# Kernel optimization log

Hardware: AMD Instinct MI355X
Metric: run time of the kernel (lower is better)

The kernel has to match this reference:

```python
import jax, jax.numpy as jnp
import numpy as np

T, H, E, I, K = 2048, 2048, 16, 512, 2
ROUTED_SCALE = 1.5   # config.moe_router_scaling_factor
SWIGLU_LIMIT = 7.0   # config.swiglu_limits[layer_id]


def setup_inputs() -> dict:
    key = jax.random.key(0)
    k1, k2, k3, k4, k5 = jax.random.split(key, 5)
    hidden_states = jax.random.normal(k1, (T, H), jnp.float32)
    gate_w = jax.random.normal(k2, (E, H), jnp.float32) * 0.02
    router_bias = jax.random.normal(k3, (E,), jnp.float32) * 0.01
    w13 = jax.random.normal(k4, (E, 2 * I, H), jnp.float32) * 0.02  # [gate; up] fused
    w2 = jax.random.normal(k5, (E, H, I), jnp.float32) * 0.02
    return {"hidden_states": hidden_states, "gate_w": gate_w,
            "router_bias": router_bias, "w13": w13, "w2": w2, "top_k": K}


def reference(hidden_states, gate_w, router_bias, w13, w2, top_k):
    n_tok = hidden_states.shape[0]
    n_exp = gate_w.shape[0]
    # fp32 gate (need_fp32_gate=True)
    router_logits = hidden_states.astype(jnp.float32) @ gate_w.T          # [T, E]
    scores = jax.nn.sigmoid(router_logits)
    # correction bias only affects expert choice, not the combine weights
    _, topk_ids = jax.lax.top_k(scores + router_bias[None, :], top_k)     # [T, K]
    topk_w = jnp.take_along_axis(scores, topk_ids, axis=1)                # [T, K]
    topk_w = topk_w / jnp.sum(topk_w, axis=1, keepdims=True)              # renormalize
    topk_w = topk_w * ROUTED_SCALE
    # scatter routing weights into dense per-expert combine weights [T, E]
    comb = jnp.zeros((n_tok, n_exp), jnp.float32)
    comb = comb.at[jnp.arange(n_tok)[:, None], topk_ids].add(topk_w)
    # expert SwiGLU MLPs, dense over experts (zero combine weight == not routed)
    gu = jnp.einsum('th,eoh->teo', hidden_states, w13)                    # [T, E, 2I]
    g, u = jnp.split(gu, 2, axis=-1)
    g = jnp.minimum(g, SWIGLU_LIMIT)                                      # gemm1_clamp_limit
    u = jnp.clip(u, -SWIGLU_LIMIT, SWIGLU_LIMIT)
    act = g * jax.nn.sigmoid(g) * u                                       # silu(gate) * up
    expert_out = jnp.einsum('tei,ehi->teh', act, w2)                      # [T, E, H]
    return jnp.einsum('teh,te->th', expert_out, comb)                     # [T, H]
```

## Files before the change

### kernel.cpp

```cpp
#include <hip/hip_runtime.h>
#include <hip/hip_bf16.h>
#include <math.h>

#define T_TOK 2048
#define H_DIM 2048
#define E_EXP 16
#define I_DIM 512
#define TWO_I 1024
#define ROUTED_SCALE 1.5f
#define SWIGLU_LIMIT 7.0f

#define BM 64
#define KC 64
#define PADMAX 5120
#define MAX_TILES 80

typedef __attribute__((ext_vector_type(8))) short bf16x8;
typedef __attribute__((ext_vector_type(4))) float f32x4;
typedef unsigned short u16;

__device__ inline u16 f2bf(float f) {
    return __builtin_bit_cast(u16, __float2bfloat16(f));
}
__device__ inline bf16x8 pack8(float4 a, float4 b) {
    bf16x8 v;
    v[0] = (short)f2bf(a.x); v[1] = (short)f2bf(a.y);
    v[2] = (short)f2bf(a.z); v[3] = (short)f2bf(a.w);
    v[4] = (short)f2bf(b.x); v[5] = (short)f2bf(b.y);
    v[6] = (short)f2bf(b.z); v[7] = (short)f2bf(b.w);
    return v;
}

#define SWZ(row, k) ((row) * 64 + ((k) ^ (((row) & 7) << 3)))

__global__ __launch_bounds__(256) void router_kernel(
    const float* __restrict__ hs, const float* __restrict__ gw,
    const float* __restrict__ bias, int* cnt, int* tok_list, float* w_list,
    u16* __restrict__ hs_bf)
{
    int wave = threadIdx.x >> 6;
    int lane = threadIdx.x & 63;
    int t = blockIdx.x * 4 + wave;
    if (t >= T_TOK) return;
    const float* x = hs + (size_t)t * H_DIM;

    float acc[E_EXP];
#pragma unroll
    for (int e = 0; e < E_EXP; ++e) acc[e] = 0.f;

#pragma unroll 2
    for (int c = 0; c < 8; ++c) {
        int col = c * 256 + lane * 4;
        float4 xv = *(const float4*)(x + col);
        ushort4 pv;
        pv.x = f2bf(xv.x); pv.y = f2bf(xv.y); pv.z = f2bf(xv.z); pv.w = f2bf(xv.w);
        *(ushort4*)(hs_bf + (size_t)t * H_DIM + col) = pv;
#pragma unroll
        for (int e = 0; e < E_EXP; ++e) {
            float4 gv = *(const float4*)(gw + (size_t)e * H_DIM + col);
            acc[e] = fmaf(xv.x, gv.x, acc[e]);
            acc[e] = fmaf(xv.y, gv.y, acc[e]);
            acc[e] = fmaf(xv.z, gv.z, acc[e]);
            acc[e] = fmaf(xv.w, gv.w, acc[e]);
        }
    }
#pragma unroll
    for (int e = 0; e < E_EXP; ++e) {
        for (int m = 32; m >= 1; m >>= 1)
            acc[e] += __shfl_xor(acc[e], m, 64);
    }
    if (lane == 0) {
        float sc[E_EXP], bsc[E_EXP];
#pragma unroll
        for (int e = 0; e < E_EXP; ++e) {
            sc[e] = 1.f / (1.f + expf(-acc[e]));
            bsc[e] = sc[e] + bias[e];
        }
        int e0 = 0; float b0 = bsc[0];
#pragma unroll
        for (int e = 1; e < E_EXP; ++e) if (bsc[e] > b0) { b0 = bsc[e]; e0 = e; }
        int e1 = -1; float b1 = -1e30f;
#pragma unroll
        for (int e = 0; e < E_EXP; ++e) {
            if (e == e0) continue;
            if (bsc[e] > b1) { b1 = bsc[e]; e1 = e; }
        }
        float s0 = sc[e0], s1 = sc[e1];
        float inv = ROUTED_SCALE / (s0 + s1);
        int p0 = atomicAdd(&cnt[e0], 1);
        tok_list[e0 * T_TOK + p0] = t;
        w_list[e0 * T_TOK + p0] = s0 * inv;
        int p1 = atomicAdd(&cnt[e1], 1);
        tok_list[e1 * T_TOK + p1] = t;
        w_list[e1 * T_TOK + p1] = s1 * inv;
    }
}

__global__ void scatter_build(const int* __restrict__ cnt,
    const int* __restrict__ tok_list, const float* __restrict__ w_list,
    int* A_tok, float* A_w, int* tile_e, int* tile_r0)
{
    int c[E_EXP], offs[E_EXP + 1];
    offs[0] = 0;
#pragma unroll
    for (int e = 0; e < E_EXP; ++e) {
        c[e] = cnt[e];
        offs[e + 1] = offs[e] + ((c[e] + BM - 1) & ~(BM - 1));
    }
    int idx = blockIdx.x * 256 + threadIdx.x;
    int e = idx >> 11;
    int pos = idx & (T_TOK - 1);
    int ce = c[e];
    int pe = (ce + BM - 1) & ~(BM - 1);
    if (pos < ce) {
        A_tok[offs[e] + pos] = tok_list[idx];
        A_w[offs[e] + pos] = w_list[idx];
    } else if (pos < pe) {
        A_tok[offs[e] + pos] = -1;
        A_w[offs[e] + pos] = 0.f;
    }
    if (idx == 0) {
        int nt = 0;
        for (int ee = 0; ee < E_EXP; ++ee) {
            int ntile = (c[ee] + BM - 1) >> 6;
            for (int j = 0; j < ntile; ++j) {
                tile_e[nt] = ee;
                tile_r0[nt] = offs[ee] + j * BM;
                ++nt;
            }
        }
        for (; nt < MAX_TILES; ++nt) tile_e[nt] = -1;
    }
}

__global__ __launch_bounds__(256, 3) void gemm1_act(
    const u16* __restrict__ hs_bf, const float* __restrict__ w13,
    const int* __restrict__ A_tok,
    const int* __restrict__ tile_e, const int* __restrict__ tile_r0,
    u16* __restrict__ act)
{
    int b = blockIdx.x;
    int id = (b & 7) * 80 + (b >> 3);
    int tile = id % MAX_TILES;
    int y = id / MAX_TILES;
    int e = tile_e[tile];
    if (e < 0) return;
    int row0 = tile_r0[tile];
    int i0 = y * 64;
    int tid = threadIdx.x;

    __shared__ u16 Xs[2][4096];
    __shared__ u16 Gs[2][4096];
    __shared__ u16 Us[2][4096];

    const int r  = tid >> 2;
    const int kq = tid & 3;
    const int tok_r = A_tok[row0 + r];
    const bool xok = tok_r >= 0;
    const u16* xsrc = hs_bf + (size_t)(xok ? tok_r : 0) * H_DIM + kq * 16;
    const float* gsrc = w13 + ((size_t)e * TWO_I + i0 + r) * H_DIM + kq * 16;
    const float* usrc = gsrc + (size_t)I_DIM * H_DIM;
    const int wb0 = SWZ(r, kq * 16);
    const int wb1 = SWZ(r, kq * 16 + 8);
    const bf16x8 BZ = {0, 0, 0, 0, 0, 0, 0, 0};

    bf16x8 xv0, xv1;
    float4 gv0, gv1, gv2, gv3, uv0, uv1, uv2, uv3;

#define G1_LOAD(t) do { int k0 = (t) * KC; \
    xv0 = xok ? *(const bf16x8*)(xsrc + k0)     : BZ; \
    xv1 = xok ? *(const bf16x8*)(xsrc + k0 + 8) : BZ; \
    gv0 = *(const float4*)(gsrc + k0);      gv1 = *(const float4*)(gsrc + k0 + 4); \
    gv2 = *(const float4*)(gsrc + k0 + 8);  gv3 = *(const float4*)(gsrc + k0 + 12); \
    uv0 = *(const float4*)(usrc + k0);      uv1 = *(const float4*)(usrc + k0 + 4); \
    uv2 = *(const float4*)(usrc + k0 + 8);  uv3 = *(const float4*)(usrc + k0 + 12); } while (0)

#define G1_WRITE(bb) do { \
    *(bf16x8*)&Xs[bb][wb0] = xv0;             *(bf16x8*)&Xs[bb][wb1] = xv1; \
    *(bf16x8*)&Gs[bb][wb0] = pack8(gv0, gv1); *(bf16x8*)&Gs[bb][wb1] = pack8(gv2, gv3); \
    *(bf16x8*)&Us[bb][wb0] = pack8(uv0, uv1); *(bf16x8*)&Us[bb][wb1] = pack8(uv2, uv3); } while (0)

    const int l  = tid & 63;
    const int w  = tid >> 6;
    const int wm = w >> 1, wn = w & 1;
    const int lr = l & 15;
    const int lg = l >> 4;
    const int ra0 = wm * 32 + lr, ra1 = ra0 + 16;
    const int rb0 = wn * 32 + lr, rb1 = rb0 + 16;
    int ia0[2], ia1[2], ib0[2], ib1[2];
#pragma unroll
    for (int kh = 0; kh < 2; ++kh) {
        int e2 = kh * 32 + lg * 8;
        ia0[kh] = SWZ(ra0, e2); ia1[kh] = SWZ(ra1, e2);
        ib0[kh] = SWZ(rb0, e2); ib1[kh] = SWZ(rb1, e2);
    }

    const f32x4 Z4 = {0.f, 0.f, 0.f, 0.f};
    f32x4 aG[2][2], aU[2][2];
#pragma unroll
    for (int m = 0; m < 2; ++m)
#pragma unroll
        for (int n = 0; n < 2; ++n) { aG[m][n] = Z4; aU[m][n] = Z4; }

    G1_LOAD(0);
    G1_WRITE(0);
    __syncthreads();
    int cur = 0;
    const int NT = H_DIM / KC;
    for (int t = 0; t < NT; ++t) {
        int tn = (t + 1 < NT) ? t + 1 : t;
        G1_LOAD(tn);
#pragma unroll
        for (int kh = 0; kh < 2; ++kh) {
            bf16x8 a0 = *(const bf16x8*)&Xs[cur][ia0[kh]];
            bf16x8 a1 = *(const bf16x8*)&Xs[cur][ia1[kh]];
            bf16x8 g0 = *(const bf16x8*)&Gs[cur][ib0[kh]];
            bf16x8 g1 = *(const bf16x8*)&Gs[cur][ib1[kh]];
            bf16x8 u0 = *(const bf16x8*)&Us[cur][ib0[kh]];
            bf16x8 u1 = *(const bf16x8*)&Us[cur][ib1[kh]];
            aG[0][0] = __builtin_amdgcn_mfma_f32_16x16x32_bf16(a0, g0, aG[0][0], 0, 0, 0);
            aG[0][1] = __builtin_amdgcn_mfma_f32_16x16x32_bf16(a0, g1, aG[0][1], 0, 0, 0);
            aG[1][0] = __builtin_amdgcn_mfma_f32_16x16x32_bf16(a1, g0, aG[1][0], 0, 0, 0);
            aG[1][1] = __builtin_amdgcn_mfma_f32_16x16x32_bf16(a1, g1, aG[1][1], 0, 0, 0);
            aU[0][0] = __builtin_amdgcn_mfma_f32_16x16x32_bf16(a0, u0, aU[0][0], 0, 0, 0);
            aU[0][1] = __builtin_amdgcn_mfma_f32_16x16x32_bf16(a0, u1, aU[0][1], 0, 0, 0);
            aU[1][0] = __builtin_amdgcn_mfma_f32_16x16x32_bf16(a1, u0, aU[1][0], 0, 0, 0);
            aU[1][1] = __builtin_amdgcn_mfma_f32_16x16x32_bf16(a1, u1, aU[1][1], 0, 0, 0);
        }
        G1_WRITE(cur ^ 1);
        __syncthreads();
        cur ^= 1;
    }
#undef G1_LOAD
#undef G1_WRITE

#pragma unroll
    for (int m = 0; m < 2; ++m)
#pragma unroll
        for (int n = 0; n < 2; ++n) {
            int col = i0 + wn * 32 + n * 16 + lr;
            int rbase = row0 + wm * 32 + m * 16 + lg * 4;
#pragma unroll
            for (int q = 0; q < 4; ++q) {
                float g = fminf(aG[m][n][q], SWIGLU_LIMIT);
                float u = fminf(fmaxf(aU[m][n][q], -SWIGLU_LIMIT), SWIGLU_LIMIT);
                float s = 1.f / (1.f + __expf(-g));
                act[(size_t)(rbase + q) * I_DIM + col] = f2bf(g * s * u);
            }
        }
}

__global__ __launch_bounds__(256, 4) void gemm2_scatter(
    const u16* __restrict__ act, const float* __restrict__ w2,
    const int* __restrict__ A_tok, const float* __restrict__ A_w,
    const int* __restrict__ tile_e, const int* __restrict__ tile_r0,
    float* __restrict__ out)
{
    int b = blockIdx.x;
    int id = (b & 7) * 320 + (b >> 3);
    int tile = id % MAX_TILES;
    int y = id / MAX_TILES;
    int e = tile_e[tile];
    if (e < 0) return;
    int row0 = tile_r0[tile];
    int h0 = y * 64;
    int tid = threadIdx.x;

    __shared__ u16 As[2][4096];
    __shared__ u16 Bs[2][4096];
    __shared__ int toks[BM];
    __shared__ float wts[BM];
    if (tid < BM) { toks[tid] = A_tok[row0 + tid]; wts[tid] = A_w[row0 + tid]; }

    const int r  = tid >> 2;
    const int kq = tid & 3;
    const u16* asrc = act + (size_t)(row0 + r) * I_DIM + kq * 16;
    const float* bsrc = w2 + ((size_t)e * H_DIM + h0 + r) * I_DIM + kq * 16;
    const int wb0 = SWZ(r, kq * 16);
    const int wb1 = SWZ(r, kq * 16 + 8);

    bf16x8 av0, av1;
    float4 bv0, bv1, bv2, bv3;

#define G2_LOAD(t) do { int k0 = (t) * KC; \
    av0 = *(const bf16x8*)(asrc + k0); av1 = *(const bf16x8*)(asrc + k0 + 8); \
    bv0 = *(const float4*)(bsrc + k0);      bv1 = *(const float4*)(bsrc + k0 + 4); \
    bv2 = *(const float4*)(bsrc + k0 + 8);  bv3 = *(const float4*)(bsrc + k0 + 12); } while (0)

#define G2_WRITE(bb) do { \
    *(bf16x8*)&As[bb][wb0] = av0;             *(bf16x8*)&As[bb][wb1] = av1; \
    *(bf16x8*)&Bs[bb][wb0] = pack8(bv0, bv1); *(bf16x8*)&Bs[bb][wb1] = pack8(bv2, bv3); } while (0)

    const int l  = tid & 63;
    const int w  = tid >> 6;
    const int wm = w >> 1, wn = w & 1;
    const int lr = l & 15;
    const int lg = l >> 4;
    const int ra0 = wm * 32 + lr, ra1 = ra0 + 16;
    const int rb0 = wn * 32 + lr, rb1 = rb0 + 16;
    int ia0[2], ia1[2], ib0[2], ib1[2];
#pragma unroll
    for (int kh = 0; kh < 2; ++kh) {
        int e2 = kh * 32 + lg * 8;
        ia0[kh] = SWZ(ra0, e2); ia1[kh] = SWZ(ra1, e2);
        ib0[kh] = SWZ(rb0, e2); ib1[kh] = SWZ(rb1, e2);
    }

    const f32x4 Z4 = {0.f, 0.f, 0.f, 0.f};
    f32x4 acc[2][2];
#pragma unroll
    for (int m = 0; m < 2; ++m)
#pragma unroll
        for (int n = 0; n < 2; ++n) acc[m][n] = Z4;

    G2_LOAD(0);
    G2_WRITE(0);
    __syncthreads();
    int cur = 0;
    const int NT = I_DIM / KC;
    for (int t = 0; t < NT; ++t) {
        int tn = (t + 1 < NT) ? t + 1 : t;
        G2_LOAD(tn);
#pragma unroll
        for (int kh = 0; kh < 2; ++kh) {
            bf16x8 a0 = *(const bf16x8*)&As[cur][ia0[kh]];
            bf16x8 a1 = *(const bf16x8*)&As[cur][ia1[kh]];
            bf16x8 b0 = *(const bf16x8*)&Bs[cur][ib0[kh]];
            bf16x8 b1 = *(const bf16x8*)&Bs[cur][ib1[kh]];
            acc[0][0] = __builtin_amdgcn_mfma_f32_16x16x32_bf16(a0, b0, acc[0][0], 0, 0, 0);
            acc[0][1] = __builtin_amdgcn_mfma_f32_16x16x32_bf16(a0, b1, acc[0][1], 0, 0, 0);
            acc[1][0] = __builtin_amdgcn_mfma_f32_16x16x32_bf16(a1, b0, acc[1][0], 0, 0, 0);
            acc[1][1] = __builtin_amdgcn_mfma_f32_16x16x32_bf16(a1, b1, acc[1][1], 0, 0, 0);
        }
        G2_WRITE(cur ^ 1);
        __syncthreads();
        cur ^= 1;
    }
#undef G2_LOAD
#undef G2_WRITE

#pragma unroll
    for (int m = 0; m < 2; ++m)
#pragma unroll
        for (int n = 0; n < 2; ++n) {
            int col = h0 + wn * 32 + n * 16 + lr;
            int sbase = wm * 32 + m * 16 + lg * 4;
#pragma unroll
            for (int q = 0; q < 4; ++q) {
                int slot = sbase + q;
                int tok = toks[slot];
                if (tok >= 0)
                    atomicAdd(&out[(size_t)tok * H_DIM + col], acc[m][n][q] * wts[slot]);
            }
        }
}

extern "C" void kernel_launch(void* const* d_in, const int* in_sizes, int n_in,
                              void* d_out, int out_size, void* d_ws, size_t ws_size,
                              hipStream_t stream) {
    const float* hs   = (const float*)d_in[0];
    const float* gw   = (const float*)d_in[1];
    const float* bias = (const float*)d_in[2];
    const float* w13  = (const float*)d_in[3];
    const float* w2   = (const float*)d_in[4];
    float* out = (float*)d_out;

    char* ws = (char*)d_ws;
    int*   cnt      = (int*)(ws + 0);
    int*   tile_e   = (int*)(ws + 64);
    int*   tile_r0  = (int*)(ws + 384);
    int*   tok_list = (int*)(ws + 1024);
    float* w_list   = (float*)(ws + 132096);
    int*   A_tok    = (int*)(ws + 263168);
    float* A_w      = (float*)(ws + 283648);
    u16*   act      = (u16*)(ws + 304128);
    u16*   hs_bf    = (u16*)(ws + 5547008);

    hipMemsetAsync(d_out, 0, (size_t)T_TOK * H_DIM * sizeof(float), stream);
    hipMemsetAsync(cnt, 0, 64, stream);

    router_kernel<<<T_TOK / 4, 256, 0, stream>>>(hs, gw, bias, cnt, tok_list, w_list, hs_bf);
    scatter_build<<<(E_EXP * T_TOK) / 256, 256, 0, stream>>>(cnt, tok_list, w_list, A_tok, A_w, tile_e, tile_r0);

    gemm1_act<<<MAX_TILES * 8, 256, 0, stream>>>(hs_bf, w13, A_tok, tile_e, tile_r0, act);
    gemm2_scatter<<<MAX_TILES * 32, 256, 0, stream>>>(act, w2, A_tok, A_w, tile_e, tile_r0, out);
}
```

Baseline: 196.5 us.

## Pre-convert expert weights to bf16 and stage GEMM tiles via direct global-to-LDS loads

Adds a kernel that converts w13 and w2 to bf16 in the workspace on every call. New GEMM variants then read the bf16 weights and use global_load_lds to copy tiles straight into swizzled shared memory, skipping the register round trip and the per-tile conversion. The aim is to halve the bytes each GEMM reads for weights and simplify the load pipeline. The cost is a full extra pass over all weights (read fp32, write bf16) each call, and the path only runs if the workspace is large enough, otherwise it falls back to the fp32 kernels.

```diff
diff --git a/kernel.cpp b/kernel.cpp
--- a/kernel.cpp
+++ b/kernel.cpp
@@ -12,7 +12,6 @@
 
 #define BM 64
 #define KC 64
-#define PADMAX 5120
 #define MAX_TILES 80
 
 typedef __attribute__((ext_vector_type(8))) short bf16x8;
@@ -31,7 +30,30 @@
     return v;
 }
 
+__device__ inline void gload16(const u16* g, u16* l) {
+    __builtin_amdgcn_global_load_lds(
+        (const __attribute__((address_space(1))) void*)(g),
+        (__attribute__((address_space(3))) void*)(l), 16, 0, 0);
+}
+
 #define SWZ(row, k) ((row) * 64 + ((k) ^ (((row) & 7) << 3)))
+
+#define NV13 4194304
+#define NVTOT 6291456
+__global__ __launch_bounds__(256) void convert_w(
+    const float* __restrict__ w13, const float* __restrict__ w2,
+    u16* __restrict__ w13b, u16* __restrict__ w2b)
+{
+    int stride = gridDim.x * 256;
+    for (size_t v = blockIdx.x * 256 + threadIdx.x; v < NVTOT; v += stride) {
+        const float* s; u16* d;
+        if (v < NV13) { s = w13 + v * 8; d = w13b + v * 8; }
+        else          { s = w2 + (v - NV13) * 8; d = w2b + (v - NV13) * 8; }
+        float4 a = *(const float4*)s;
+        float4 b = *(const float4*)(s + 4);
+        *(bf16x8*)d = pack8(a, b);
+    }
+}
 
 __global__ __launch_bounds__(256) void router_kernel(
     const float* __restrict__ hs, const float* __restrict__ gw,
@@ -133,11 +155,11 @@
     }
 }
 
-__global__ __launch_bounds__(256, 3) void gemm1_act(
-    const u16* __restrict__ hs_bf, const float* __restrict__ w13,
-    const int* __restrict__ A_tok,
-    const int* __restrict__ tile_e, const int* __restrict__ tile_r0,
-    u16* __restrict__ act)
+
+__global__ __launch_bounds__(256, 3) void gemm1_bf(
+    const u16* __restrict__ hs_bf, const u16* __restrict__ w13b,
+    const int* __restrict__ A_tok, const int* __restrict__ tile_e,
+    const int* __restrict__ tile_r0, u16* __restrict__ act)
 {
     int b = blockIdx.x;
     int id = (b & 7) * 80 + (b >> 3);
@@ -153,35 +175,27 @@
     __shared__ u16 Gs[2][4096];
     __shared__ u16 Us[2][4096];
 
-    const int r  = tid >> 2;
-    const int kq = tid & 3;
-    const int tok_r = A_tok[row0 + r];
-    const bool xok = tok_r >= 0;
-    const u16* xsrc = hs_bf + (size_t)(xok ? tok_r : 0) * H_DIM + kq * 16;
-    const float* gsrc = w13 + ((size_t)e * TWO_I + i0 + r) * H_DIM + kq * 16;
-    const float* usrc = gsrc + (size_t)I_DIM * H_DIM;
-    const int wb0 = SWZ(r, kq * 16);
-    const int wb1 = SWZ(r, kq * 16 + 8);
-    const bf16x8 BZ = {0, 0, 0, 0, 0, 0, 0, 0};
-
-    bf16x8 xv0, xv1;
-    float4 gv0, gv1, gv2, gv3, uv0, uv1, uv2, uv3;
-
-#define G1_LOAD(t) do { int k0 = (t) * KC; \
-    xv0 = xok ? *(const bf16x8*)(xsrc + k0)     : BZ; \
-    xv1 = xok ? *(const bf16x8*)(xsrc + k0 + 8) : BZ; \
-    gv0 = *(const float4*)(gsrc + k0);      gv1 = *(const float4*)(gsrc + k0 + 4); \
-    gv2 = *(const float4*)(gsrc + k0 + 8);  gv3 = *(const float4*)(gsrc + k0 + 12); \
-    uv0 = *(const float4*)(usrc + k0);      uv1 = *(const float4*)(usrc + k0 + 4); \
-    uv2 = *(const float4*)(usrc + k0 + 8);  uv3 = *(const float4*)(usrc + k0 + 12); } while (0)
-
-#define G1_WRITE(bb) do { \
-    *(bf16x8*)&Xs[bb][wb0] = xv0;             *(bf16x8*)&Xs[bb][wb1] = xv1; \
-    *(bf16x8*)&Gs[bb][wb0] = pack8(gv0, gv1); *(bf16x8*)&Gs[bb][wb1] = pack8(gv2, gv3); \
-    *(bf16x8*)&Us[bb][wb0] = pack8(uv0, uv1); *(bf16x8*)&Us[bb][wb1] = pack8(uv2, uv3); } while (0)
-
-    const int l  = tid & 63;
-    const int w  = tid >> 6;
+    const int l = tid & 63, w = tid >> 6;
+    const int rlo = l >> 3;
+    const int c8 = (l & 7) << 3;
+    const int ksrc = c8 ^ (rlo << 3);
+    const int rowA = w * 16 + rlo;
+    const int rowB = rowA + 8;
+    int tokA = A_tok[row0 + rowA]; if (tokA < 0) tokA = 0;
+    int tokB = A_tok[row0 + rowB]; if (tokB < 0) tokB = 0;
+    const u16* sXA = hs_bf + (size_t)tokA * H_DIM + ksrc;
+    const u16* sXB = hs_bf + (size_t)tokB * H_DIM + ksrc;
+    const u16* sGA = w13b + ((size_t)e * TWO_I + i0 + rowA) * H_DIM + ksrc;
+    const u16* sGB = sGA + 8 * H_DIM;
+    const u16* sUA = sGA + (size_t)I_DIM * H_DIM;
+    const u16* sUB = sUA + 8 * H_DIM;
+    const int dA = w * 1024;
+
+#define G1STAGE(bb, t) do { int ko = (t) * KC; \
+    gload16(sXA + ko, &Xs[bb][dA]);  gload16(sXB + ko, &Xs[bb][dA + 512]); \
+    gload16(sGA + ko, &Gs[bb][dA]);  gload16(sGB + ko, &Gs[bb][dA + 512]); \
+    gload16(sUA + ko, &Us[bb][dA]);  gload16(sUB + ko, &Us[bb][dA + 512]); } while (0)
+
     const int wm = w >> 1, wn = w & 1;
     const int lr = l & 15;
     const int lg = l >> 4;
@@ -202,14 +216,12 @@
 #pragma unroll
         for (int n = 0; n < 2; ++n) { aG[m][n] = Z4; aU[m][n] = Z4; }
 
-    G1_LOAD(0);
-    G1_WRITE(0);
+    G1STAGE(0, 0);
     __syncthreads();
     int cur = 0;
     const int NT = H_DIM / KC;
     for (int t = 0; t < NT; ++t) {
-        int tn = (t + 1 < NT) ? t + 1 : t;
-        G1_LOAD(tn);
+        if (t + 1 < NT) G1STAGE(cur ^ 1, t + 1);
 #pragma unroll
         for (int kh = 0; kh < 2; ++kh) {
             bf16x8 a0 = *(const bf16x8*)&Xs[cur][ia0[kh]];
@@ -227,12 +239,10 @@
             aU[1][0] = __builtin_amdgcn_mfma_f32_16x16x32_bf16(a1, u0, aU[1][0], 0, 0, 0);
             aU[1][1] = __builtin_amdgcn_mfma_f32_16x16x32_bf16(a1, u1, aU[1][1], 0, 0, 0);
         }
-        G1_WRITE(cur ^ 1);
         __syncthreads();
         cur ^= 1;
     }
-#undef G1_LOAD
-#undef G1_WRITE
+#undef G1STAGE
 
 #pragma unroll
     for (int m = 0; m < 2; ++m)
@@ -250,7 +260,220 @@
         }
 }
 
-__global__ __launch_bounds__(256, 4) void gemm2_scatter(
+__global__ __launch_bounds__(256, 4) void gemm2_bf(
+    const u16* __restrict__ act, const u16* __restrict__ w2b,
+    const int* __restrict__ A_tok, const float* __restrict__ A_w,
+    const int* __restrict__ tile_e, const int* __restrict__ tile_r0,
+    float* __restrict__ out)
+{
+    int b = blockIdx.x;
+    int id = (b & 7) * 320 + (b >> 3);
+    int tile = id % MAX_TILES;
+    int y = id / MAX_TILES;
+    int e = tile_e[tile];
+    if (e < 0) return;
+    int row0 = tile_r0[tile];
+    int h0 = y * 64;
+    int tid = threadIdx.x;
+
+    __shared__ u16 As[2][4096];
+    __shared__ u16 Bs[2][4096];
+    __shared__ int toks[BM];
+    __shared__ float wts[BM];
+    if (tid < BM) { toks[tid] = A_tok[row0 + tid]; wts[tid] = A_w[row0 + tid]; }
+
+    const int l = tid & 63, w = tid >> 6;
+    const int rlo = l >> 3;
+    const int c8 = (l & 7) << 3;
+    const int ksrc = c8 ^ (rlo << 3);
+    const int rowA = w * 16 + rlo;
+    const int rowB = rowA + 8;
+    const u16* sAA = act + (size_t)(row0 + rowA) * I_DIM + ksrc;
+    const u16* sAB = act + (size_t)(row0 + rowB) * I_DIM + ksrc;
+    const u16* sBA = w2b + ((size_t)e * H_DIM + h0 + rowA) * I_DIM + ksrc;
+    const u16* sBB = sBA + 8 * I_DIM;
+    const int dA = w * 1024;
+
+#define G2STAGE(bb, t) do { int ko = (t) * KC; \
+    gload16(sAA + ko, &As[bb][dA]);  gload16(sAB + ko, &As[bb][dA + 512]); \
+    gload16(sBA + ko, &Bs[bb][dA]);  gload16(sBB + ko, &Bs[bb][dA + 512]); } while (0)
+
+    const int wm = w >> 1, wn = w & 1;
+    const int lr = l & 15;
+    const int lg = l >> 4;
+    const int ra0 = wm * 32 + lr, ra1 = ra0 + 16;
+    const int rb0 = wn * 32 + lr, rb1 = rb0 + 16;
+    int ia0[2], ia1[2], ib0[2], ib1[2];
+#pragma unroll
+    for (int kh = 0; kh < 2; ++kh) {
+        int e2 = kh * 32 + lg * 8;
+        ia0[kh] = SWZ(ra0, e2); ia1[kh] = SWZ(ra1, e2);
+        ib0[kh] = SWZ(rb0, e2); ib1[kh] = SWZ(rb1, e2);
+    }
+
+    const f32x4 Z4 = {0.f, 0.f, 0.f, 0.f};
+    f32x4 acc[2][2];
+#pragma unroll
+    for (int m = 0; m < 2; ++m)
+#pragma unroll
+        for (int n = 0; n < 2; ++n) acc[m][n] = Z4;
+
+    G2STAGE(0, 0);
+    __syncthreads();
+    int cur = 0;
+    const int NT = I_DIM / KC;
+    for (int t = 0; t < NT; ++t) {
+        if (t + 1 < NT) G2STAGE(cur ^ 1, t + 1);
+#pragma unroll
+        for (int kh = 0; kh < 2; ++kh) {
+            bf16x8 a0 = *(const bf16x8*)&As[cur][ia0[kh]];
+            bf16x8 a1 = *(const bf16x8*)&As[cur][ia1[kh]];
+            bf16x8 b0 = *(const bf16x8*)&Bs[cur][ib0[kh]];
+            bf16x8 b1 = *(const bf16x8*)&Bs[cur][ib1[kh]];
+            acc[0][0] = __builtin_amdgcn_mfma_f32_16x16x32_bf16(a0, b0, acc[0][0], 0, 0, 0);
+            acc[0][1] = __builtin_amdgcn_mfma_f32_16x16x32_bf16(a0, b1, acc[0][1], 0, 0, 0);
+            acc[1][0] = __builtin_amdgcn_mfma_f32_16x16x32_bf16(a1, b0, acc[1][0], 0, 0, 0);
+            acc[1][1] = __builtin_amdgcn_mfma_f32_16x16x32_bf16(a1, b1, acc[1][1], 0, 0, 0);
+        }
+        __syncthreads();
+        cur ^= 1;
+    }
+#undef G2STAGE
+
+#pragma unroll
+    for (int m = 0; m < 2; ++m)
+#pragma unroll
+        for (int n = 0; n < 2; ++n) {
+            int col = h0 + wn * 32 + n * 16 + lr;
+            int sbase = wm * 32 + m * 16 + lg * 4;
+#pragma unroll
+            for (int q = 0; q < 4; ++q) {
+                int slot = sbase + q;
+                int tok = toks[slot];
+                if (tok >= 0)
+                    atomicAdd(&out[(size_t)tok * H_DIM + col], acc[m][n][q] * wts[slot]);
+            }
+        }
+}
+
+
+__global__ __launch_bounds__(256, 3) void gemm1_f32(
+    const u16* __restrict__ hs_bf, const float* __restrict__ w13,
+    const int* __restrict__ A_tok,
+    const int* __restrict__ tile_e, const int* __restrict__ tile_r0,
+    u16* __restrict__ act)
+{
+    int b = blockIdx.x;
+    int id = (b & 7) * 80 + (b >> 3);
+    int tile = id % MAX_TILES;
+    int y = id / MAX_TILES;
+    int e = tile_e[tile];
+    if (e < 0) return;
+    int row0 = tile_r0[tile];
+    int i0 = y * 64;
+    int tid = threadIdx.x;
+
+    __shared__ u16 Xs[2][4096];
+    __shared__ u16 Gs[2][4096];
+    __shared__ u16 Us[2][4096];
+
+    const int r  = tid >> 2;
+    const int kq = tid & 3;
+    const int tok_r = A_tok[row0 + r];
+    const bool xok = tok_r >= 0;
+    const u16* xsrc = hs_bf + (size_t)(xok ? tok_r : 0) * H_DIM + kq * 16;
+    const float* gsrc = w13 + ((size_t)e * TWO_I + i0 + r) * H_DIM + kq * 16;
+    const float* usrc = gsrc + (size_t)I_DIM * H_DIM;
+    const int wb0 = SWZ(r, kq * 16);
+    const int wb1 = SWZ(r, kq * 16 + 8);
+    const bf16x8 BZ = {0, 0, 0, 0, 0, 0, 0, 0};
+
+    bf16x8 xv0, xv1;
+    float4 gv0, gv1, gv2, gv3, uv0, uv1, uv2, uv3;
+
+#define G1_LOAD(t) do { int k0 = (t) * KC; \
+    xv0 = xok ? *(const bf16x8*)(xsrc + k0)     : BZ; \
+    xv1 = xok ? *(const bf16x8*)(xsrc + k0 + 8) : BZ; \
+    gv0 = *(const float4*)(gsrc + k0);      gv1 = *(const float4*)(gsrc + k0 + 4); \
+    gv2 = *(const float4*)(gsrc + k0 + 8);  gv3 = *(const float4*)(gsrc + k0 + 12); \
+    uv0 = *(const float4*)(usrc + k0);      uv1 = *(const float4*)(usrc + k0 + 4); \
+    uv2 = *(const float4*)(usrc + k0 + 8);  uv3 = *(const float4*)(usrc + k0 + 12); } while (0)
+#define G1_WRITE(bb) do { \
+    *(bf16x8*)&Xs[bb][wb0] = xv0;             *(bf16x8*)&Xs[bb][wb1] = xv1; \
+    *(bf16x8*)&Gs[bb][wb0] = pack8(gv0, gv1); *(bf16x8*)&Gs[bb][wb1] = pack8(gv2, gv3); \
+    *(bf16x8*)&Us[bb][wb0] = pack8(uv0, uv1); *(bf16x8*)&Us[bb][wb1] = pack8(uv2, uv3); } while (0)
+
+    const int l  = tid & 63;
+    const int w  = tid >> 6;
+    const int wm = w >> 1, wn = w & 1;
+    const int lr = l & 15;
+    const int lg = l >> 4;
+    const int ra0 = wm * 32 + lr, ra1 = ra0 + 16;
+    const int rb0 = wn * 32 + lr, rb1 = rb0 + 16;
+    int ia0[2], ia1[2], ib0[2], ib1[2];
+#pragma unroll
+    for (int kh = 0; kh < 2; ++kh) {
+        int e2 = kh * 32 + lg * 8;
+        ia0[kh] = SWZ(ra0, e2); ia1[kh] = SWZ(ra1, e2);
+        ib0[kh] = SWZ(rb0, e2); ib1[kh] = SWZ(rb1, e2);
+    }
+
+    const f32x4 Z4 = {0.f, 0.f, 0.f, 0.f};
+    f32x4 aG[2][2], aU[2][2];
+#pragma unroll
+    for (int m = 0; m < 2; ++m)
+#pragma unroll
+        for (int n = 0; n < 2; ++n) { aG[m][n] = Z4; aU[m][n] = Z4; }
+
+    G1_LOAD(0);
+    G1_WRITE(0);
+    __syncthreads();
+    int cur = 0;
+    const int NT = H_DIM / KC;
+    for (int t = 0; t < NT; ++t) {
+        int tn = (t + 1 < NT) ? t + 1 : t;
+        G1_LOAD(tn);
+#pragma unroll
+        for (int kh = 0; kh < 2; ++kh) {
+            bf16x8 a0 = *(const bf16x8*)&Xs[cur][ia0[kh]];
+            bf16x8 a1 = *(const bf16x8*)&Xs[cur][ia1[kh]];
+            bf16x8 g0 = *(const bf16x8*)&Gs[cur][ib0[kh]];
+            bf16x8 g1 = *(const bf16x8*)&Gs[cur][ib1[kh]];
+            bf16x8 u0 = *(const bf16x8*)&Us[cur][ib0[kh]];
+            bf16x8 u1 = *(const bf16x8*)&Us[cur][ib1[kh]];
+            aG[0][0] = __builtin_amdgcn_mfma_f32_16x16x32_bf16(a0, g0, aG[0][0], 0, 0, 0);
+            aG[0][1] = __builtin_amdgcn_mfma_f32_16x16x32_bf16(a0, g1, aG[0][1], 0, 0, 0);
+            aG[1][0] = __builtin_amdgcn_mfma_f32_16x16x32_bf16(a1, g0, aG[1][0], 0, 0, 0);
+            aG[1][1] = __builtin_amdgcn_mfma_f32_16x16x32_bf16(a1, g1, aG[1][1], 0, 0, 0);
+            aU[0][0] = __builtin_amdgcn_mfma_f32_16x16x32_bf16(a0, u0, aU[0][0], 0, 0, 0);
+            aU[0][1] = __builtin_amdgcn_mfma_f32_16x16x32_bf16(a0, u1, aU[0][1], 0, 0, 0);
+            aU[1][0] = __builtin_amdgcn_mfma_f32_16x16x32_bf16(a1, u0, aU[1][0], 0, 0, 0);
+            aU[1][1] = __builtin_amdgcn_mfma_f32_16x16x32_bf16(a1, u1, aU[1][1], 0, 0, 0);
+        }
+        G1_WRITE(cur ^ 1);
+        __syncthreads();
+        cur ^= 1;
+    }
+#undef G1_LOAD
+#undef G1_WRITE
+
+#pragma unroll
+    for (int m = 0; m < 2; ++m)
+#pragma unroll
+        for (int n = 0; n < 2; ++n) {
+            int col = i0 + wn * 32 + n * 16 + lr;
+            int rbase = row0 + wm * 32 + m * 16 + lg * 4;
+#pragma unroll
+            for (int q = 0; q < 4; ++q) {
+                float g = fminf(aG[m][n][q], SWIGLU_LIMIT);
+                float u = fminf(fmaxf(aU[m][n][q], -SWIGLU_LIMIT), SWIGLU_LIMIT);
+                float s = 1.f / (1.f + __expf(-g));
+                act[(size_t)(rbase + q) * I_DIM + col] = f2bf(g * s * u);
+            }
+        }
+}
+
+__global__ __launch_bounds__(256, 4) void gemm2_f32(
     const u16* __restrict__ act, const float* __restrict__ w2,
     const int* __restrict__ A_tok, const float* __restrict__ A_w,
     const int* __restrict__ tile_e, const int* __restrict__ tile_r0,
@@ -286,7 +509,6 @@
     av0 = *(const bf16x8*)(asrc + k0); av1 = *(const bf16x8*)(asrc + k0 + 8); \
     bv0 = *(const float4*)(bsrc + k0);      bv1 = *(const float4*)(bsrc + k0 + 4); \
     bv2 = *(const float4*)(bsrc + k0 + 8);  bv3 = *(const float4*)(bsrc + k0 + 12); } while (0)
-
 #define G2_WRITE(bb) do { \
     *(bf16x8*)&As[bb][wb0] = av0;             *(bf16x8*)&As[bb][wb1] = av1; \
     *(bf16x8*)&Bs[bb][wb0] = pack8(bv0, bv1); *(bf16x8*)&Bs[bb][wb1] = pack8(bv2, bv3); } while (0)
@@ -375,13 +597,25 @@
     float* A_w      = (float*)(ws + 283648);
     u16*   act      = (u16*)(ws + 304128);
     u16*   hs_bf    = (u16*)(ws + 5547008);
+    u16*   w13b     = (u16*)(ws + 13935616);
+    u16*   w2b      = (u16*)(ws + 81044480);
+    const size_t NEED_BF = 114598912;
+    const bool bf_path = ws_size >= NEED_BF;
 
     hipMemsetAsync(d_out, 0, (size_t)T_TOK * H_DIM * sizeof(float), stream);
     hipMemsetAsync(cnt, 0, 64, stream);
 
+    if (bf_path)
+        convert_w<<<3072, 256, 0, stream>>>(w13, w2, w13b, w2b);
+
     router_kernel<<<T_TOK / 4, 256, 0, stream>>>(hs, gw, bias, cnt, tok_list, w_list, hs_bf);
     scatter_build<<<(E_EXP * T_TOK) / 256, 256, 0, stream>>>(cnt, tok_list, w_list, A_tok, A_w, tile_e, tile_r0);
 
-    gemm1_act<<<MAX_TILES * 8, 256, 0, stream>>>(hs_bf, w13, A_tok, tile_e, tile_r0, act);
-    gemm2_scatter<<<MAX_TILES * 32, 256, 0, stream>>>(act, w2, A_tok, A_w, tile_e, tile_r0, out);
-}
+    if (bf_path) {
+        gemm1_bf<<<MAX_TILES * 8, 256, 0, stream>>>(hs_bf, w13b, A_tok, tile_e, tile_r0, act);
+        gemm2_bf<<<MAX_TILES * 32, 256, 0, stream>>>(act, w2b, A_tok, A_w, tile_e, tile_r0, out);
+    } else {
+        gemm1_f32<<<MAX_TILES * 8, 256, 0, stream>>>(hs_bf, w13, A_tok, tile_e, tile_r0, act);
+        gemm2_f32<<<MAX_TILES * 32, 256, 0, stream>>>(act, w2, A_tok, A_w, tile_e, tile_r0, out);
+    }
+}
```

Result: slower. 227.2 us (+15.7%).

## Stage bf16 activations via direct global-to-LDS loads and coalesce fp32 weight loads

Applied to the files above, without the earlier changes.

Both GEMM kernels now stage the bf16 activation tile straight into LDS with global_load_lds, pre-swizzling the source address so the LDS layout matches the existing XOR swizzle. The fp32 weight loads are remapped so 16 threads cover one contiguous row segment, which improves coalescing and changes the LDS stores to 4-element chunks. The loop also skips the redundant final prefetch, adds a sched_barrier, and lowers gemm2's occupancy hint from 4 to 3. Padded token rows now load token 0's data instead of zeros. That relies on the scatter step skipping negative tokens, and it may break if gemm1 results for padded rows are consumed without masking.

```diff
diff --git a/kernel.cpp b/kernel.cpp
--- a/kernel.cpp
+++ b/kernel.cpp
@@ -12,7 +12,6 @@
 
 #define BM 64
 #define KC 64
-#define PADMAX 5120
 #define MAX_TILES 80
 
 typedef __attribute__((ext_vector_type(8))) short bf16x8;
@@ -22,13 +21,16 @@
 __device__ inline u16 f2bf(float f) {
     return __builtin_bit_cast(u16, __float2bfloat16(f));
 }
-__device__ inline bf16x8 pack8(float4 a, float4 b) {
-    bf16x8 v;
-    v[0] = (short)f2bf(a.x); v[1] = (short)f2bf(a.y);
-    v[2] = (short)f2bf(a.z); v[3] = (short)f2bf(a.w);
-    v[4] = (short)f2bf(b.x); v[5] = (short)f2bf(b.y);
-    v[6] = (short)f2bf(b.z); v[7] = (short)f2bf(b.w);
+__device__ inline ushort4 pack4(float4 a) {
+    ushort4 v;
+    v.x = f2bf(a.x); v.y = f2bf(a.y); v.z = f2bf(a.z); v.w = f2bf(a.w);
     return v;
+}
+
+__device__ inline void gload16(const u16* g, u16* l) {
+    __builtin_amdgcn_global_load_lds(
+        (const __attribute__((address_space(1))) void*)(g),
+        (__attribute__((address_space(3))) void*)(l), 16, 0, 0);
 }
 
 #define SWZ(row, k) ((row) * 64 + ((k) ^ (((row) & 7) << 3)))
@@ -52,9 +54,7 @@
     for (int c = 0; c < 8; ++c) {
         int col = c * 256 + lane * 4;
         float4 xv = *(const float4*)(x + col);
-        ushort4 pv;
-        pv.x = f2bf(xv.x); pv.y = f2bf(xv.y); pv.z = f2bf(xv.z); pv.w = f2bf(xv.w);
-        *(ushort4*)(hs_bf + (size_t)t * H_DIM + col) = pv;
+        *(ushort4*)(hs_bf + (size_t)t * H_DIM + col) = pack4(xv);
 #pragma unroll
         for (int e = 0; e < E_EXP; ++e) {
             float4 gv = *(const float4*)(gw + (size_t)e * H_DIM + col);
@@ -135,9 +135,8 @@
 
 __global__ __launch_bounds__(256, 3) void gemm1_act(
     const u16* __restrict__ hs_bf, const float* __restrict__ w13,
-    const int* __restrict__ A_tok,
-    const int* __restrict__ tile_e, const int* __restrict__ tile_r0,
-    u16* __restrict__ act)
+    const int* __restrict__ A_tok, const int* __restrict__ tile_e,
+    const int* __restrict__ tile_r0, u16* __restrict__ act)
 {
     int b = blockIdx.x;
     int id = (b & 7) * 80 + (b >> 3);
@@ -153,35 +152,50 @@
     __shared__ u16 Gs[2][4096];
     __shared__ u16 Us[2][4096];
 
-    const int r  = tid >> 2;
-    const int kq = tid & 3;
-    const int tok_r = A_tok[row0 + r];
-    const bool xok = tok_r >= 0;
-    const u16* xsrc = hs_bf + (size_t)(xok ? tok_r : 0) * H_DIM + kq * 16;
-    const float* gsrc = w13 + ((size_t)e * TWO_I + i0 + r) * H_DIM + kq * 16;
+    const int l = tid & 63, w = tid >> 6;
+
+    const int rlo = l >> 3;
+    const int c8 = (l & 7) << 3;
+    const int ksrc = c8 ^ (rlo << 3);
+    const int rowA = w * 16 + rlo;
+    const int rowB = rowA + 8;
+    int tokA = A_tok[row0 + rowA]; if (tokA < 0) tokA = 0;
+    int tokB = A_tok[row0 + rowB]; if (tokB < 0) tokB = 0;
+    const u16* sXA = hs_bf + (size_t)tokA * H_DIM + ksrc;
+    const u16* sXB = hs_bf + (size_t)tokB * H_DIM + ksrc;
+    const int dA = w * 1024;
+
+#define X_STAGE(bb, t) do { int ko = (t) * KC; \
+    gload16(sXA + ko, &Xs[bb][dA]);  gload16(sXB + ko, &Xs[bb][dA + 512]); } while (0)
+
+    const int srow = tid >> 4;
+    const int sc4  = tid & 15;
+    const int kphys = (sc4 * 4) ^ ((srow & 7) << 3);
+    const int sbase = srow * 64 + kphys;
+    const float* gsrc = w13 + ((size_t)e * TWO_I + i0 + srow) * H_DIM + sc4 * 4;
     const float* usrc = gsrc + (size_t)I_DIM * H_DIM;
-    const int wb0 = SWZ(r, kq * 16);
-    const int wb1 = SWZ(r, kq * 16 + 8);
-    const bf16x8 BZ = {0, 0, 0, 0, 0, 0, 0, 0};
-
-    bf16x8 xv0, xv1;
-    float4 gv0, gv1, gv2, gv3, uv0, uv1, uv2, uv3;
-
-#define G1_LOAD(t) do { int k0 = (t) * KC; \
-    xv0 = xok ? *(const bf16x8*)(xsrc + k0)     : BZ; \
-    xv1 = xok ? *(const bf16x8*)(xsrc + k0 + 8) : BZ; \
-    gv0 = *(const float4*)(gsrc + k0);      gv1 = *(const float4*)(gsrc + k0 + 4); \
-    gv2 = *(const float4*)(gsrc + k0 + 8);  gv3 = *(const float4*)(gsrc + k0 + 12); \
-    uv0 = *(const float4*)(usrc + k0);      uv1 = *(const float4*)(usrc + k0 + 4); \
-    uv2 = *(const float4*)(usrc + k0 + 8);  uv3 = *(const float4*)(usrc + k0 + 12); } while (0)
-
-#define G1_WRITE(bb) do { \
-    *(bf16x8*)&Xs[bb][wb0] = xv0;             *(bf16x8*)&Xs[bb][wb1] = xv1; \
-    *(bf16x8*)&Gs[bb][wb0] = pack8(gv0, gv1); *(bf16x8*)&Gs[bb][wb1] = pack8(gv2, gv3); \
-    *(bf16x8*)&Us[bb][wb0] = pack8(uv0, uv1); *(bf16x8*)&Us[bb][wb1] = pack8(uv2, uv3); } while (0)
-
-    const int l  = tid & 63;
-    const int w  = tid >> 6;
+
+    float4 gld[4], uld[4];
+#define W_LOAD(t) do { int k0 = (t) * KC; \
+    gld[0] = *(const float4*)(gsrc + k0); \
+    gld[1] = *(const float4*)(gsrc + k0 + 16 * H_DIM); \
+    gld[2] = *(const float4*)(gsrc + k0 + 32 * H_DIM); \
+    gld[3] = *(const float4*)(gsrc + k0 + 48 * H_DIM); \
+    uld[0] = *(const float4*)(usrc + k0); \
+    uld[1] = *(const float4*)(usrc + k0 + 16 * H_DIM); \
+    uld[2] = *(const float4*)(usrc + k0 + 32 * H_DIM); \
+    uld[3] = *(const float4*)(usrc + k0 + 48 * H_DIM); } while (0)
+
+#define W_WRITE(bb) do { \
+    *(ushort4*)&Gs[bb][sbase]        = pack4(gld[0]); \
+    *(ushort4*)&Gs[bb][sbase + 1024] = pack4(gld[1]); \
+    *(ushort4*)&Gs[bb][sbase + 2048] = pack4(gld[2]); \
+    *(ushort4*)&Gs[bb][sbase + 3072] = pack4(gld[3]); \
+    *(ushort4*)&Us[bb][sbase]        = pack4(uld[0]); \
+    *(ushort4*)&Us[bb][sbase + 1024] = pack4(uld[1]); \
+    *(ushort4*)&Us[bb][sbase + 2048] = pack4(uld[2]); \
+    *(ushort4*)&Us[bb][sbase + 3072] = pack4(uld[3]); } while (0)
+
     const int wm = w >> 1, wn = w & 1;
     const int lr = l & 15;
     const int lg = l >> 4;
@@ -202,14 +216,19 @@
 #pragma unroll
         for (int n = 0; n < 2; ++n) { aG[m][n] = Z4; aU[m][n] = Z4; }
 
-    G1_LOAD(0);
-    G1_WRITE(0);
+    W_LOAD(0);
+    X_STAGE(0, 0);
+    W_WRITE(0);
     __syncthreads();
     int cur = 0;
     const int NT = H_DIM / KC;
     for (int t = 0; t < NT; ++t) {
-        int tn = (t + 1 < NT) ? t + 1 : t;
-        G1_LOAD(tn);
+        const bool more = (t + 1 < NT);
+        if (more) {
+            X_STAGE(cur ^ 1, t + 1);
+            W_LOAD(t + 1);
+            __builtin_amdgcn_sched_barrier(0);
+        }
 #pragma unroll
         for (int kh = 0; kh < 2; ++kh) {
             bf16x8 a0 = *(const bf16x8*)&Xs[cur][ia0[kh]];
@@ -227,12 +246,13 @@
             aU[1][0] = __builtin_amdgcn_mfma_f32_16x16x32_bf16(a1, u0, aU[1][0], 0, 0, 0);
             aU[1][1] = __builtin_amdgcn_mfma_f32_16x16x32_bf16(a1, u1, aU[1][1], 0, 0, 0);
         }
-        G1_WRITE(cur ^ 1);
+        if (more) W_WRITE(cur ^ 1);
         __syncthreads();
         cur ^= 1;
     }
-#undef G1_LOAD
-#undef G1_WRITE
+#undef X_STAGE
+#undef W_LOAD
+#undef W_WRITE
 
 #pragma unroll
     for (int m = 0; m < 2; ++m)
@@ -250,7 +270,7 @@
         }
 }
 
-__global__ __launch_bounds__(256, 4) void gemm2_scatter(
+__global__ __launch_bounds__(256, 3) void gemm2_scatter(
     const u16* __restrict__ act, const float* __restrict__ w2,
     const int* __restrict__ A_tok, const float* __restrict__ A_w,
     const int* __restrict__ tile_e, const int* __restrict__ tile_r0,
@@ -272,27 +292,39 @@
     __shared__ float wts[BM];
     if (tid < BM) { toks[tid] = A_tok[row0 + tid]; wts[tid] = A_w[row0 + tid]; }
 
-    const int r  = tid >> 2;
-    const int kq = tid & 3;
-    const u16* asrc = act + (size_t)(row0 + r) * I_DIM + kq * 16;
-    const float* bsrc = w2 + ((size_t)e * H_DIM + h0 + r) * I_DIM + kq * 16;
-    const int wb0 = SWZ(r, kq * 16);
-    const int wb1 = SWZ(r, kq * 16 + 8);
-
-    bf16x8 av0, av1;
-    float4 bv0, bv1, bv2, bv3;
-
-#define G2_LOAD(t) do { int k0 = (t) * KC; \
-    av0 = *(const bf16x8*)(asrc + k0); av1 = *(const bf16x8*)(asrc + k0 + 8); \
-    bv0 = *(const float4*)(bsrc + k0);      bv1 = *(const float4*)(bsrc + k0 + 4); \
-    bv2 = *(const float4*)(bsrc + k0 + 8);  bv3 = *(const float4*)(bsrc + k0 + 12); } while (0)
-
-#define G2_WRITE(bb) do { \
-    *(bf16x8*)&As[bb][wb0] = av0;             *(bf16x8*)&As[bb][wb1] = av1; \
-    *(bf16x8*)&Bs[bb][wb0] = pack8(bv0, bv1); *(bf16x8*)&Bs[bb][wb1] = pack8(bv2, bv3); } while (0)
-
-    const int l  = tid & 63;
-    const int w  = tid >> 6;
+    const int l = tid & 63, w = tid >> 6;
+
+    const int rlo = l >> 3;
+    const int c8 = (l & 7) << 3;
+    const int ksrc = c8 ^ (rlo << 3);
+    const int rowA = w * 16 + rlo;
+    const int rowB = rowA + 8;
+    const u16* sAA = act + (size_t)(row0 + rowA) * I_DIM + ksrc;
+    const u16* sAB = act + (size_t)(row0 + rowB) * I_DIM + ksrc;
+    const int dA = w * 1024;
+
+#define A_STAGE(bb, t) do { int ko = (t) * KC; \
+    gload16(sAA + ko, &As[bb][dA]);  gload16(sAB + ko, &As[bb][dA + 512]); } while (0)
+
+    const int srow = tid >> 4;
+    const int sc4  = tid & 15;
+    const int kphys = (sc4 * 4) ^ ((srow & 7) << 3);
+    const int sbase = srow * 64 + kphys;
+    const float* bsrc = w2 + ((size_t)e * H_DIM + h0 + srow) * I_DIM + sc4 * 4;
+
+    float4 bld[4];
+#define B_LOAD(t) do { int k0 = (t) * KC; \
+    bld[0] = *(const float4*)(bsrc + k0); \
+    bld[1] = *(const float4*)(bsrc + k0 + 16 * I_DIM); \
+    bld[2] = *(const float4*)(bsrc + k0 + 32 * I_DIM); \
+    bld[3] = *(const float4*)(bsrc + k0 + 48 * I_DIM); } while (0)
+
+#define B_WRITE(bb) do { \
+    *(ushort4*)&Bs[bb][sbase]        = pack4(bld[0]); \
+    *(ushort4*)&Bs[bb][sbase + 1024] = pack4(bld[1]); \
+    *(ushort4*)&Bs[bb][sbase + 2048] = pack4(bld[2]); \
+    *(ushort4*)&Bs[bb][sbase + 3072] = pack4(bld[3]); } while (0)
+
     const int wm = w >> 1, wn = w & 1;
     const int lr = l & 15;
     const int lg = l >> 4;
@@ -313,14 +345,19 @@
 #pragma unroll
         for (int n = 0; n < 2; ++n) acc[m][n] = Z4;
 
-    G2_LOAD(0);
-    G2_WRITE(0);
+    B_LOAD(0);
+    A_STAGE(0, 0);
+    B_WRITE(0);
     __syncthreads();
     int cur = 0;
     const int NT = I_DIM / KC;
     for (int t = 0; t < NT; ++t) {
-        int tn = (t + 1 < NT) ? t + 1 : t;
-        G2_LOAD(tn);
+        const bool more = (t + 1 < NT);
+        if (more) {
+            A_STAGE(cur ^ 1, t + 1);
+            B_LOAD(t + 1);
+            __builtin_amdgcn_sched_barrier(0);
+        }
 #pragma unroll
         for (int kh = 0; kh < 2; ++kh) {
             bf16x8 a0 = *(const bf16x8*)&As[cur][ia0[kh]];
@@ -332,22 +369,23 @@
             acc[1][0] = __builtin_amdgcn_mfma_f32_16x16x32_bf16(a1, b0, acc[1][0], 0, 0, 0);
             acc[1][1] = __builtin_amdgcn_mfma_f32_16x16x32_bf16(a1, b1, acc[1][1], 0, 0, 0);
         }
-        G2_WRITE(cur ^ 1);
+        if (more) B_WRITE(cur ^ 1);
         __syncthreads();
         cur ^= 1;
     }
-#undef G2_LOAD
-#undef G2_WRITE
+#undef A_STAGE
+#undef B_LOAD
+#undef B_WRITE
 
 #pragma unroll
     for (int m = 0; m < 2; ++m)
 #pragma unroll
         for (int n = 0; n < 2; ++n) {
             int col = h0 + wn * 32 + n * 16 + lr;
-            int sbase = wm * 32 + m * 16 + lg * 4;
+            int sbase2 = wm * 32 + m * 16 + lg * 4;
 #pragma unroll
             for (int q = 0; q < 4; ++q) {
-                int slot = sbase + q;
+                int slot = sbase2 + q;
                 int tok = toks[slot];
                 if (tok >= 0)
                     atomicAdd(&out[(size_t)tok * H_DIM + col], acc[m][n][q] * wts[slot]);
```

New measurement: 178.0 us. 1.1x faster.
